# Kernel tuning notes

Hardware: AMD Instinct MI355X
Metric: run time of the kernel (lower is better)

## Reference

```python
import jax, jax.numpy as jnp
import numpy as np

P, N, C, F = 3, 50000, 5, 68   # planes, nodes/plane, classes, in+node feats
E = 150000                     # edges/plane
EF, NF = 64, 64                # edge_features, node_features

def setup_inputs() -> dict:
    key = jax.random.key(0)
    ks = jax.random.split(key, 10)
    s = 0.1
    return {
        "x": jax.random.normal(ks[0], (P, N, C, F), jnp.float32),
        "edge_index": jax.random.randint(ks[1], (P, 2, E), 0, N, jnp.int64),
        "ew1": s * jax.random.normal(ks[2], (P, C, 2 * F, EF), jnp.float32),
        "eb1": s * jax.random.normal(ks[3], (P, C, EF), jnp.float32),
        "ew2": s * jax.random.normal(ks[4], (P, C, EF, 1), jnp.float32),
        "eb2": s * jax.random.normal(ks[5], (P, C, 1), jnp.float32),
        "nw1": s * jax.random.normal(ks[6], (P, C, 2 * F, NF), jnp.float32),
        "nb1": s * jax.random.normal(ks[7], (P, C, NF), jnp.float32),
        "nw2": s * jax.random.normal(ks[8], (P, C, NF, NF), jnp.float32),
        "nb2": s * jax.random.normal(ks[9], (P, C, NF), jnp.float32),
    }

def _plane(x, ei, ew1, eb1, ew2, eb2, nw1, nb1, nw2, nb2):
    # x: [N, C, F]; ei: [2, E]
    src, dst = ei[0], ei[1]
    x_j = x[src]                                   # [E, C, F] (source)
    x_i = x[dst]                                   # [E, C, F] (target)
    # edge net input is detached in the original module
    e_in = jax.lax.stop_gradient(jnp.concatenate([x_i, x_j], axis=-1))  # [E, C, 2F]
    h = jnp.tanh(jnp.einsum('ecf,cfo->eco', e_in, ew1) + eb1)           # [E, C, EF]
    logit = jnp.einsum('ecf,cfo->eco', h, ew2) + eb2                    # [E, C, 1]
    w = jax.nn.softmax(logit, axis=1)              # softmax over classes
    msg = w * x_j                                  # [E, C, F]
    aggr = jax.ops.segment_sum(msg, dst, num_segments=x.shape[0])       # [N, C, F]
    u_in = jnp.concatenate([x, aggr], axis=-1)     # [N, C, 2F]
    h2 = jnp.tanh(jnp.einsum('ncf,cfo->nco', u_in, nw1) + nb1)          # [N, C, NF]
    return jnp.tanh(jnp.einsum('ncf,cfo->nco', h2, nw2) + nb2)          # [N, C, NF]

def reference(x, edge_index, ew1, eb1, ew2, eb2, nw1, nb1, nw2, nb2):
    return jax.vmap(_plane)(x, edge_index, ew1, eb1, ew2, eb2, nw1, nb1, nw2, nb2)
```

## Files before the change

kernel.cpp:

```cpp
#include <hip/hip_runtime.h>
#include <hip/hip_fp16.h>
#include <math.h>

typedef unsigned int uint;
typedef __fp16 half2_t __attribute__((ext_vector_type(2)));
typedef _Float16 v8h __attribute__((ext_vector_type(8)));
typedef _Float16 v4h __attribute__((ext_vector_type(4)));
typedef float f32v4 __attribute__((ext_vector_type(4)));

#define NUM_P 3
#define NUM_N 50000
#define NUM_C 5
#define NUM_E 150000
#define CF 340
#define NB32 1563
#define TE 128
#define EB2 1172
#define TN 128
#define NB128 391
#define SROW 129
#define NSB 196
#define NSBP 50176

#define AH_T   ((size_t)NUM_P * NUM_N * 170)
#define NW1_T  (NUM_P * NUM_C * 68 * 64)
#define NW2_T  (NUM_P * NUM_C * 32 * 64)
#define LG_T   ((size_t)NUM_P * NUM_C * NUM_E)
#define EWB_T  (NUM_P * NUM_C * 2 * 4 * 640)

__device__ __forceinline__ float fast_tanh(float x) {
    float a = __expf(2.0f * x);
    float t = __builtin_amdgcn_rcpf(a + 1.0f);
    return fmaf(-2.0f, t, 1.0f);
}

__device__ __forceinline__ float dot2f(half2_t a, half2_t b, float c) {
#if __has_builtin(__builtin_amdgcn_fdot2)
    return __builtin_amdgcn_fdot2(a, b, c, false);
#else
    return fmaf((float)a[0], (float)b[0], fmaf((float)a[1], (float)b[1], c));
#endif
}

__device__ __forceinline__ half2_t bc(uint u) { return __builtin_bit_cast(half2_t, u); }

__device__ __forceinline__ uint pk2(float a, float b) {
    half2_t h = __builtin_amdgcn_cvt_pkrtz(a, b);
    return __builtin_bit_cast(uint, h);
}

__global__ __launch_bounds__(256) void convert_x_kernel(
    const float4* __restrict__ x4, uint* __restrict__ xh,
    uint* __restrict__ xn, int write_xn)
{
    __shared__ uint lds[32 * 170];
    const int nb = blockIdx.x % NB32;
    const int p  = blockIdx.x / NB32;
    const int n0 = nb * 32;
    const int nvalid = (n0 + 32 <= NUM_N) ? 32 : (NUM_N - n0);
    const int t = threadIdx.x;

    const float4* src = x4 + ((size_t)p * NUM_N + n0) * 85;
    const int nf4 = nvalid * 85;
    #pragma unroll
    for (int it = 0; it < 11; ++it) {
        const int i = t + it * 256;
        if (i < nf4) {
            const float4 v = src[i];
            lds[2 * i]     = pk2(v.x, v.y);
            lds[2 * i + 1] = pk2(v.z, v.w);
        }
    }
    __syncthreads();

    const int nq = nvalid * 34;
    #pragma unroll 1
    for (int c = 0; c < NUM_C; ++c) {
        uint* dst = xh + ((size_t)(p * NUM_C + c) * NUM_N + n0) * 34;
        #pragma unroll
        for (int it = 0; it < 5; ++it) {
            const int i = t + it * 256;
            if (i < nq) {
                const int nl = i / 34, j = i - nl * 34;
                dst[i] = lds[nl * 170 + c * 34 + j];
            }
        }
    }

    if (write_xn) {
        uint* dstn = xn + ((size_t)p * NUM_N + n0) * 170;
        const int tot = nvalid * 170;
        #pragma unroll
        for (int it = 0; it < 22; ++it) {
            const int i = t + it * 256;
            if (i < tot) dstn[i] = lds[i];
        }
    }
}

__global__ __launch_bounds__(256) void pack_pairs_kernel(
    const float* __restrict__ in, uint* __restrict__ outp, int total)
{
    int i = blockIdx.x * 256 + threadIdx.x;
    if (i >= total) return;
    int t = i >> 6, o = i & 63;
    outp[i] = pk2(in[t * 128 + o], in[t * 128 + 64 + o]);
}

__global__ __launch_bounds__(256) void pack_edge_mfma_kernel(
    const float* __restrict__ ew1, uint* __restrict__ ewb)
{
    int i = blockIdx.x * 256 + threadIdx.x;
    if (i >= EWB_T) return;
    int g    = i / 5120;
    int rem  = i - g * 5120;
    int s    = rem / 2560;
    int rem2 = rem - s * 2560;
    int nt   = rem2 / 640;
    int u    = rem2 - nt * 640;

    int f0, o; bool valid;
    if (u < 512) {
        int kt = u >> 8, uu = u & 255;
        int lane = uu >> 2, pp = uu & 3;
        f0 = kt * 32 + (lane >> 4) * 8 + 2 * pp;
        o  = nt * 16 + (lane & 15);
        valid = true;
    } else {
        int uu = u - 512;
        int lane = uu >> 1, pp = uu & 1;
        f0 = 64 + (lane >> 4) * 4 + 2 * pp;
        o  = nt * 16 + (lane & 15);
        valid = ((lane >> 4) == 0);
    }
    float w0 = 0.f, w1 = 0.f;
    if (valid) {
        int f = s * 68 + f0;
        w0 = ew1[((size_t)g * 136 + f) * 64 + o];
        w1 = ew1[((size_t)g * 136 + f + 1) * 64 + o];
    }
    ewb[i] = pk2(w0, w1);
}

__global__ __launch_bounds__(128) void edge_mfma_kernel(
    const uint*  __restrict__ xh,
    const int*   __restrict__ ei,
    const uint*  __restrict__ ewb,
    const float* __restrict__ eb1,
    const float* __restrict__ ew2,
    const float* __restrict__ eb2,
    float*       __restrict__ logits)
{
    __shared__ uint smem[TE * 40];
    __shared__ int  ids[2][TE];

    const int g    = blockIdx.x / EB2;
    const int blk  = blockIdx.x - g * EB2;
    const int p    = g / NUM_C;
    const int e0   = blk * TE;
    const int t    = threadIdx.x;
    const int lane = t & 63;
    const int wv   = t >> 6;
    const int col  = lane & 15;
    const int G    = lane >> 4;

    {
        const int e  = e0 + t;
        const int ec = (e < NUM_E) ? e : (NUM_E - 1);
        ids[0][t] = ei[(p * 2 + 0) * NUM_E + ec];
        ids[1][t] = ei[(p * 2 + 1) * NUM_E + ec];
    }
    {
        const uint2 z = make_uint2(0u, 0u);
        *(uint2*)&smem[t * 40 + 34] = z;
        *(uint2*)&smem[t * 40 + 36] = z;
        *(uint2*)&smem[t * 40 + 38] = z;
    }

    const uint* slice = xh + (size_t)g * NUM_N * 34;

    float b1v[4], w2v[4];
    #pragma unroll
    for (int nt = 0; nt < 4; ++nt) {
        b1v[nt] = eb1[g * 64 + nt * 16 + col];
        w2v[nt] = ew2[g * 64 + nt * 16 + col];
    }

    f32v4 acc[4][4];
    #pragma unroll
    for (int m = 0; m < 4; ++m)
        #pragma unroll
        for (int nt = 0; nt < 4; ++nt) {
            f32v4 a = {b1v[nt], b1v[nt], b1v[nt], b1v[nt]};
            acc[m][nt] = a;
        }
    __syncthreads();

    #pragma unroll 1
    for (int side = 0; side < 2; ++side) {
        const int* idr = ids[1 - side];
        #pragma unroll
        for (int k = 0; k < 17; ++k) {
            const int i2 = t + TE * k;
            const int e  = i2 / 17, j2 = i2 - e * 17;
            const uint2 v = *(const uint2*)(slice + (size_t)idr[e] * 34 + 2 * j2);
            *(uint2*)&smem[e * 40 + 2 * j2] = v;
        }
        __syncthreads();

        const uint* wb = ewb + (size_t)((g * 2 + side) * 4) * 640;
        v8h B0[4], B1[4]; v4h B2[4];
        #pragma unroll
        for (int nt = 0; nt < 4; ++nt) {
            const uint* fb = wb + nt * 640;
            B0[nt] = __builtin_bit_cast(v8h, *(const uint4*)(fb + lane * 4));
            B1[nt] = __builtin_bit_cast(v8h, *(const uint4*)(fb + 256 + lane * 4));
            B2[nt] = __builtin_bit_cast(v4h, *(const uint2*)(fb + 512 + lane * 2));
        }

        #pragma unroll
        for (int m = 0; m < 4; ++m) {
            const uint* rp = &smem[(wv * 64 + m * 16 + col) * 40];
            const v8h A0 = __builtin_bit_cast(v8h, *(const uint4*)(rp + G * 4));
            const v8h A1 = __builtin_bit_cast(v8h, *(const uint4*)(rp + 16 + G * 4));
            const v4h A2 = __builtin_bit_cast(v4h, *(const uint2*)(rp + 32 + G * 2));
            #pragma unroll
            for (int nt = 0; nt < 4; ++nt) {
                acc[m][nt] = __builtin_amdgcn_mfma_f32_16x16x32_f16(A0, B0[nt], acc[m][nt], 0, 0, 0);
                acc[m][nt] = __builtin_amdgcn_mfma_f32_16x16x32_f16(A1, B1[nt], acc[m][nt], 0, 0, 0);
                acc[m][nt] = __builtin_amdgcn_mfma_f32_16x16x16f16(A2, B2[nt], acc[m][nt], 0, 0, 0);
            }
        }
        __syncthreads();
    }

    float* elds = (float*)smem;
    #pragma unroll
    for (int m = 0; m < 4; ++m) {
        #pragma unroll
        for (int r = 0; r < 4; ++r) {
            float part = 0.f;
            #pragma unroll
            for (int nt = 0; nt < 4; ++nt)
                part = fmaf(w2v[nt], fast_tanh(acc[m][nt][r]), part);
            elds[(wv * 64 + m * 16 + G * 4 + r) * 20 + col] = part;
        }
    }
    const float4 s0 = *(const float4*)&elds[t * 20 + 0];
    const float4 s1 = *(const float4*)&elds[t * 20 + 4];
    const float4 s2 = *(const float4*)&elds[t * 20 + 8];
    const float4 s3 = *(const float4*)&elds[t * 20 + 12];
    float lg = ((s0.x + s0.y) + (s0.z + s0.w)) + ((s1.x + s1.y) + (s1.z + s1.w))
             + ((s2.x + s2.y) + (s2.z + s2.w)) + ((s3.x + s3.y) + (s3.z + s3.w))
             + eb2[g];
    if (e0 + t < NUM_E) logits[(size_t)g * NUM_E + e0 + t] = lg;
}

__global__ __launch_bounds__(256) void deg_kernel(
    const int* __restrict__ ei, int* __restrict__ deg)
{
    const int i = blockIdx.x * 256 + threadIdx.x;
    if (i >= NUM_P * NUM_E) return;
    const int p = i / NUM_E, e = i - p * NUM_E;
    const int dst = ei[(p * 2 + 1) * NUM_E + e];
    atomicAdd(&deg[p * NUM_N + dst], 1);
}

__global__ __launch_bounds__(256) void scan_block_kernel(
    const int* __restrict__ deg, int* __restrict__ intra, int* __restrict__ bsum)
{
    __shared__ int s[256];
    const int blk = blockIdx.x % NSB;
    const int p   = blockIdx.x / NSB;
    const int t   = threadIdx.x;
    const int n   = blk * 256 + t;
    const int d   = (n < NUM_N) ? deg[p * NUM_N + n] : 0;
    s[t] = d;
    __syncthreads();
    #pragma unroll
    for (int o = 1; o < 256; o <<= 1) {
        int v = (t >= o) ? s[t - o] : 0;
        __syncthreads();
        s[t] += v;
        __syncthreads();
    }
    if (n < NUM_N) intra[p * NSBP + n] = s[t] - d;
    if (t == 255) bsum[p * NSB + blk] = s[255];
}

__global__ __launch_bounds__(256) void scan_seg_kernel(
    const int* __restrict__ bsum, int* __restrict__ segoff)
{
    __shared__ int s[256];
    const int t = threadIdx.x;
    #pragma unroll 1
    for (int p = 0; p < NUM_P; ++p) {
        const int b = (t < NSB) ? bsum[p * NSB + t] : 0;
        s[t] = b;
        __syncthreads();
        #pragma unroll
        for (int o = 1; o < 256; o <<= 1) {
            int v = (t >= o) ? s[t - o] : 0;
            __syncthreads();
            s[t] += v;
            __syncthreads();
        }
        if (t < NSB) segoff[p * NSB + t] = s[t] - b;
        __syncthreads();
    }
}

__global__ __launch_bounds__(256) void fill_kernel(
    const int* __restrict__ ei, int* __restrict__ cursor,
    const int* __restrict__ intra, const int* __restrict__ segoff,
    int* __restrict__ csr_src, int* __restrict__ csr_eid)
{
    const int i = blockIdx.x * 256 + threadIdx.x;
    if (i >= NUM_P * NUM_E) return;
    const int p = i / NUM_E, e = i - p * NUM_E;
    const int src = ei[(p * 2 + 0) * NUM_E + e];
    const int dst = ei[(p * 2 + 1) * NUM_E + e];
    const int slot = atomicAdd(&cursor[p * NUM_N + dst], 1);
    const int pos  = segoff[p * NSB + (dst >> 8)] + intra[p * NSBP + dst] + slot;
    csr_src[(size_t)p * NUM_E + pos] = src;
    csr_eid[(size_t)p * NUM_E + pos] = e;
}

__global__ __launch_bounds__(256) void gather_kernel(
    const uint*  __restrict__ xn,
    const float* __restrict__ logits,
    const int*   __restrict__ csr_src,
    const int*   __restrict__ csr_eid,
    const int*   __restrict__ deg,
    const int*   __restrict__ intra,
    const int*   __restrict__ segoff,
    uint*        __restrict__ aggr)
{
    const int wslot = threadIdx.x >> 6;
    const int lane  = threadIdx.x & 63;
    const int gw = blockIdx.x * 4 + wslot;
    const int p  = gw / NUM_N;
    const int n  = gw - p * NUM_N;

    const int dg   = deg[p * NUM_N + n];
    const int off0 = segoff[p * NSB + (n >> 8)] + intra[p * NSBP + n];

    const int q1 = lane + 64, q2 = lane + 128;
    const int c0 = lane / 34;
    const int c1 = q1 / 34;
    const int c2 = q2 / 34;

    float a0 = 0.f, a1 = 0.f, a2 = 0.f, a3 = 0.f, a4 = 0.f, a5 = 0.f;

    #pragma unroll 1
    for (int d = 0; d < dg; ++d) {
        const int src = csr_src[(size_t)p * NUM_E + off0 + d];
        const int e   = csr_eid[(size_t)p * NUM_E + off0 + d];

        float l[NUM_C];
        #pragma unroll
        for (int c = 0; c < NUM_C; ++c)
            l[c] = logits[(size_t)(p * NUM_C + c) * NUM_E + e];
        float m = l[0];
        #pragma unroll
        for (int c = 1; c < NUM_C; ++c) m = fmaxf(m, l[c]);
        float s = 0.f;
        #pragma unroll
        for (int c = 0; c < NUM_C; ++c) { l[c] = __expf(l[c] - m); s += l[c]; }
        const float inv = __builtin_amdgcn_rcpf(s);
        const float wt0 = l[0] * inv, wt1 = l[1] * inv, wt2 = l[2] * inv,
                    wt3 = l[3] * inv, wt4 = l[4] * inv;

        const float wa = (c0 == 0) ? wt0 : wt1;
        const float wb = (c1 == 1) ? wt1 : (c1 == 2) ? wt2 : wt3;
        const float wc = (c2 == 3) ? wt3 : wt4;

        const uint* row = xn + (size_t)(p * NUM_N + src) * 170;
        const uint u0 = row[lane];
        const uint u1 = row[q1];
        const uint u2 = (lane < 42) ? row[q2] : 0u;
        const half2_t h0 = bc(u0), h1 = bc(u1), h2 = bc(u2);
        a0 = fmaf(wa, (float)h0[0], a0);
        a1 = fmaf(wa, (float)h0[1], a1);
        a2 = fmaf(wb, (float)h1[0], a2);
        a3 = fmaf(wb, (float)h1[1], a3);
        a4 = fmaf(wc, (float)h2[0], a4);
        a5 = fmaf(wc, (float)h2[1], a5);
    }

    const int i0 = lane - c0 * 34;
    const int i1 = q1 - c1 * 34;
    const int i2 = q2 - c2 * 34;
    aggr[((size_t)(p * NUM_C + c0) * NUM_N + n) * 34 + i0] = pk2(a0, a1);
    aggr[((size_t)(p * NUM_C + c1) * NUM_N + n) * 34 + i1] = pk2(a2, a3);
    if (lane < 42)
        aggr[((size_t)(p * NUM_C + c2) * NUM_N + n) * 34 + i2] = pk2(a4, a5);
}

__global__ __launch_bounds__(256) void edge_scatter_kernel(
    const uint*  __restrict__ xh,
    const int*   __restrict__ ei,
    const float* __restrict__ logits,
    uint*        __restrict__ aggr)
{
    const int wslot = threadIdx.x >> 6;
    const int lane  = threadIdx.x & 63;
    const int gw    = blockIdx.x * 4 + wslot;
    const int p     = gw / NUM_E;
    const int e     = gw - p * NUM_E;

    const int src = ei[(p * 2 + 0) * NUM_E + e];
    const int dst = ei[(p * 2 + 1) * NUM_E + e];

    float l[NUM_C];
    #pragma unroll
    for (int c = 0; c < NUM_C; ++c)
        l[c] = logits[(size_t)(p * NUM_C + c) * NUM_E + e];
    float m = l[0];
    #pragma unroll
    for (int c = 1; c < NUM_C; ++c) m = fmaxf(m, l[c]);
    float s = 0.f;
    #pragma unroll
    for (int c = 0; c < NUM_C; ++c) { l[c] = __expf(l[c] - m); s += l[c]; }
    const float inv = __builtin_amdgcn_rcpf(s);
    const float wt0 = l[0] * inv, wt1 = l[1] * inv, wt2 = l[2] * inv,
                wt3 = l[3] * inv, wt4 = l[4] * inv;

    #pragma unroll
    for (int k = 0; k < 3; ++k) {
        const int q = lane + 64 * k;
        if (q < 170) {
            const int c   = q / 34;
            const int idx = q - c * 34;
            const float wv = (c == 0) ? wt0 : (c == 1) ? wt1 : (c == 2) ? wt2
                           : (c == 3) ? wt3 : wt4;
            const uint xv = xh[((size_t)(p * NUM_C + c) * NUM_N + src) * 34 + idx];
            half2_t mv = __builtin_amdgcn_cvt_pkrtz(wv, wv) * bc(xv);
            uint* ap = aggr + ((size_t)(p * NUM_C + c) * NUM_N + dst) * 34 + idx;
            unsafeAtomicAdd((__half2*)ap, __builtin_bit_cast(__half2, mv));
        }
    }
}

__device__ __forceinline__ void dot_side(const uint* __restrict__ xp,
                                         const uint* __restrict__ wp,
                                         float acc[64])
{
    uint2 cur = *(const uint2*)(xp);
    #pragma unroll 1
    for (int j = 0; j < 17; ++j) {
        const int jn = (j < 16) ? (j + 1) : 16;
        const uint2 nxt = *(const uint2*)(xp + jn * 2);
        const half2_t a0 = bc(cur.x);
        const half2_t a1 = bc(cur.y);
        const uint* w0 = wp + (2 * j) * 64;
        #pragma unroll
        for (int o = 0; o < 64; ++o)
            acc[o] = dot2f(a0, bc(w0[o]), acc[o]);
        const uint* w1 = w0 + 64;
        #pragma unroll
        for (int o = 0; o < 64; ++o)
            acc[o] = dot2f(a1, bc(w1[o]), acc[o]);
        cur = nxt;
    }
}

__device__ __forceinline__ void dot_side_f32(const float* __restrict__ xf,
                                             const uint* __restrict__ wp,
                                             float acc[64])
{
    float4 cur = *(const float4*)(xf);
    #pragma unroll 1
    for (int j = 0; j < 17; ++j) {
        const int jn = (j < 16) ? (j + 1) : 16;
        const float4 nxt = *(const float4*)(xf + jn * 4);
        const half2_t a0 = __builtin_amdgcn_cvt_pkrtz(cur.x, cur.y);
        const half2_t a1 = __builtin_amdgcn_cvt_pkrtz(cur.z, cur.w);
        const uint* w0 = wp + (2 * j) * 64;
        #pragma unroll
        for (int o = 0; o < 64; ++o)
            acc[o] = dot2f(a0, bc(w0[o]), acc[o]);
        const uint* w1 = w0 + 64;
        #pragma unroll
        for (int o = 0; o < 64; ++o)
            acc[o] = dot2f(a1, bc(w1[o]), acc[o]);
        cur = nxt;
    }
}

__global__ __launch_bounds__(128) void node_kernel(
    const float* __restrict__ x,
    const uint*  __restrict__ xh,
    const uint*  __restrict__ aggr,
    const uint*  __restrict__ nwp,
    const uint*  __restrict__ n2p,
    const float* __restrict__ nb1,
    const float* __restrict__ nb2,
    float*       __restrict__ out,
    int use_xh)
{
    __shared__ uint buf[34][SROW];

    const int g   = blockIdx.x / NB128;
    const int blk = blockIdx.x - g * NB128;
    const int p   = g / NUM_C;
    const int c   = g - p * NUM_C;
    const int n0  = blk * TN;
    const int t   = threadIdx.x;
    const int nvalid = (n0 + TN <= NUM_N) ? TN : (NUM_N - n0);
    const int lim2 = nvalid * 17;

    float acc[64];
    const float* b1 = nb1 + g * 64;
    #pragma unroll
    for (int o4 = 0; o4 < 64; o4 += 4) {
        const float4 bv = *(const float4*)(b1 + o4);
        acc[o4] = bv.x; acc[o4 + 1] = bv.y; acc[o4 + 2] = bv.z; acc[o4 + 3] = bv.w;
    }
    const uint* wg = nwp + (size_t)g * 68 * 64;

    if (use_xh) {
        const uint* srcp = xh + ((size_t)g * NUM_N + n0) * 34;
        #pragma unroll
        for (int k = 0; k < 17; ++k) {
            const int i2  = t + TN * k;
            const int i2c = (i2 < lim2) ? i2 : (lim2 - 1);
            const uint2 v = *(const uint2*)(srcp + 2 * i2c);
            const int nl = i2 / 17, j2 = i2 - nl * 17;
            buf[2 * j2][nl]     = v.x;
            buf[2 * j2 + 1][nl] = v.y;
        }
    } else {
        #pragma unroll
        for (int k = 0; k < 34; ++k) {
            const int i  = t + TN * k;
            const int nl = i / 34, j = i - nl * 34;
            const int nn = (nl < nvalid) ? (n0 + nl) : n0;
            const float2 v = *(const float2*)(x + ((size_t)p * NUM_N + nn) * CF
                                              + c * 68 + 2 * j);
            buf[j][nl] = pk2(v.x, v.y);
        }
    }
    __syncthreads();
    #pragma unroll 1
    for (int j = 0; j < 34; ++j) {
        const half2_t a = bc(buf[j][t]);
        const uint* w = wg + j * 64;
        #pragma unroll
        for (int o = 0; o < 64; ++o) acc[o] = dot2f(a, bc(w[o]), acc[o]);
    }
    __syncthreads();

    {
        const uint* srcp = aggr + ((size_t)g * NUM_N + n0) * 34;
        #pragma unroll
        for (int k = 0; k < 17; ++k) {
            const int i2  = t + TN * k;
            const int i2c = (i2 < lim2) ? i2 : (lim2 - 1);
            const uint2 v = *(const uint2*)(srcp + 2 * i2c);
            const int nl = i2 / 17, j2 = i2 - nl * 17;
            buf[2 * j2][nl]     = v.x;
            buf[2 * j2 + 1][nl] = v.y;
        }
    }
    __syncthreads();
    #pragma unroll 1
    for (int j = 0; j < 34; ++j) {
        const half2_t a = bc(buf[j][t]);
        const uint* w = wg + (34 + j) * 64;
        #pragma unroll
        for (int o = 0; o < 64; ++o) acc[o] = dot2f(a, bc(w[o]), acc[o]);
    }

    uint h2p[32];
    #pragma unroll
    for (int f2 = 0; f2 < 32; ++f2)
        h2p[f2] = pk2(fast_tanh(acc[2 * f2]), fast_tanh(acc[2 * f2 + 1]));

    const float* b2 = nb2 + g * 64;
    float acc2[64];
    #pragma unroll
    for (int o4 = 0; o4 < 64; o4 += 4) {
        const float4 bv = *(const float4*)(b2 + o4);
        acc2[o4] = bv.x; acc2[o4 + 1] = bv.y; acc2[o4 + 2] = bv.z; acc2[o4 + 3] = bv.w;
    }
    const uint* w2g = n2p + (size_t)g * 32 * 64;
    #pragma unroll
    for (int f2 = 0; f2 < 32; ++f2) {
        const half2_t hv = bc(h2p[f2]);
        const uint* wr = w2g + f2 * 64;
        #pragma unroll
        for (int o = 0; o < 64; ++o)
            acc2[o] = dot2f(hv, bc(wr[o]), acc2[o]);
    }

    if (t < nvalid) {
        float* op = out + ((size_t)(p * NUM_N + n0 + t) * NUM_C + c) * 64;
        #pragma unroll
        for (int o4 = 0; o4 < 64; o4 += 4) {
            float4 ov;
            ov.x = fast_tanh(acc2[o4 + 0]);
            ov.y = fast_tanh(acc2[o4 + 1]);
            ov.z = fast_tanh(acc2[o4 + 2]);
            ov.w = fast_tanh(acc2[o4 + 3]);
            *(float4*)(op + o4) = ov;
        }
    }
}

extern "C" void kernel_launch(void* const* d_in, const int* in_sizes, int n_in,
                              void* d_out, int out_size, void* d_ws, size_t ws_size,
                              hipStream_t stream)
{
    (void)in_sizes; (void)n_in; (void)out_size;

    const float* x   = (const float*)d_in[0];
    const int*   ei  = (const int*)  d_in[1];
    const float* ew1 = (const float*)d_in[2];
    const float* eb1 = (const float*)d_in[3];
    const float* ew2 = (const float*)d_in[4];
    const float* eb2 = (const float*)d_in[5];
    const float* nw1 = (const float*)d_in[6];
    const float* nb1 = (const float*)d_in[7];
    const float* nw2 = (const float*)d_in[8];
    const float* nb2 = (const float*)d_in[9];
    float*       out = (float*)d_out;

    uint* ws     = (uint*)d_ws;
    uint* aggr_h = ws;
    uint* nwp    = ws + AH_T;
    uint* n2p    = nwp + NW1_T;
    const size_t o_xh = AH_T + NW1_T + NW2_T;
    const bool fits = ws_size >= (o_xh + AH_T) * sizeof(uint);
    uint*  xh     = fits ? (ws + o_xh) : (uint*)d_out;
    uint*  xn     = (uint*)d_out;
    float* logits = (float*)((uint*)d_out + AH_T);
    uint*  ewb    = (uint*)d_out + AH_T + LG_T;

    int* ibase   = (int*)(ewb + EWB_T);
    int* deg     = ibase;
    int* cursor  = ibase + NUM_P * NUM_N;
    int* intra   = cursor + NUM_P * NUM_N;
    int* bsum    = intra + NUM_P * NSBP;
    int* segoff  = bsum + NUM_P * NSB;
    int* csr_src = segoff + NUM_P * NSB;
    int* csr_eid = csr_src + NUM_P * NUM_E;

    convert_x_kernel<<<NUM_P * NB32, 256, 0, stream>>>(
        (const float4*)x, xh, xn, fits ? 1 : 0);
    pack_edge_mfma_kernel<<<(EWB_T + 255) / 256, 256, 0, stream>>>(ew1, ewb);
    pack_pairs_kernel<<<(NW1_T + 255) / 256, 256, 0, stream>>>(nw1, nwp, NW1_T);
    pack_pairs_kernel<<<(NW2_T + 255) / 256, 256, 0, stream>>>(nw2, n2p, NW2_T);

    edge_mfma_kernel<<<NUM_P * NUM_C * EB2, 128, 0, stream>>>(
        xh, ei, ewb, eb1, ew2, eb2, logits);

    if (fits) {
        (void)hipMemsetAsync(ibase, 0, (size_t)2 * NUM_P * NUM_N * sizeof(int), stream);
        const int egrid = (NUM_P * NUM_E + 255) / 256;
        deg_kernel<<<egrid, 256, 0, stream>>>(ei, deg);
        scan_block_kernel<<<NUM_P * NSB, 256, 0, stream>>>(deg, intra, bsum);
        scan_seg_kernel<<<1, 256, 0, stream>>>(bsum, segoff);
        fill_kernel<<<egrid, 256, 0, stream>>>(ei, cursor, intra, segoff,
                                               csr_src, csr_eid);
        gather_kernel<<<(NUM_P * NUM_N) / 4, 256, 0, stream>>>(
            xn, logits, csr_src, csr_eid, deg, intra, segoff, aggr_h);
    } else {
        (void)hipMemsetAsync(aggr_h, 0, AH_T * sizeof(uint), stream);
        edge_scatter_kernel<<<(NUM_P * NUM_E) / 4, 256, 0, stream>>>(
            xh, ei, logits, aggr_h);
    }

    node_kernel<<<NUM_P * NUM_C * NB128, 128, 0, stream>>>(
        x, xh, aggr_h, nwp, n2p, nb1, nb2, out, fits ? 1 : 0);
}
```

Baseline: 668.7 us.

## Port node MLP to MFMA matrix instructions with LDS-staged tiles

Adds a node kernel that computes both node-MLP layers with f16 MFMA instructions instead of per-thread dot2 loops. Node features and aggregates are staged in padded LDS rows, the first layer's hidden activations are written back to LDS as f16, and the output goes through an LDS transpose for coalesced stores. The goal is to turn the compute-bound scalar dot products into matrix-core throughput. In exchange it adds LDS traffic and extra synchronisation, and the new path only runs when the CSR path is selected.

```diff
diff --git a/kernel.cpp b/kernel.cpp
--- a/kernel.cpp
+++ b/kernel.cpp
@@ -49,6 +49,11 @@
     return __builtin_bit_cast(uint, h);
 }
 
+__device__ __forceinline__ v8h mk8(uint a, uint b, uint c, uint d) {
+    uint4 u; u.x = a; u.y = b; u.z = c; u.w = d;
+    return __builtin_bit_cast(v8h, u);
+}
+
 __global__ __launch_bounds__(256) void convert_x_kernel(
     const float4* __restrict__ x4, uint* __restrict__ xh,
     uint* __restrict__ xn, int write_xn)
@@ -442,6 +447,164 @@
     }
 }
 
+__global__ __launch_bounds__(128) void node_mfma_kernel(
+    const uint*  __restrict__ xh,
+    const uint*  __restrict__ aggr,
+    const uint*  __restrict__ nwp,
+    const uint*  __restrict__ n2p,
+    const float* __restrict__ nb1,
+    const float* __restrict__ nb2,
+    float*       __restrict__ out)
+{
+    __shared__ uint smem[TN * 40];
+
+    const int g    = blockIdx.x / NB128;
+    const int blk  = blockIdx.x - g * NB128;
+    const int p    = g / NUM_C;
+    const int c    = g - p * NUM_C;
+    const int n0   = blk * TN;
+    const int t    = threadIdx.x;
+    const int lane = t & 63;
+    const int wv   = t >> 6;
+    const int col  = lane & 15;
+    const int G    = lane >> 4;
+    const int nvalid = (n0 + TN <= NUM_N) ? TN : (NUM_N - n0);
+    const int lim2   = nvalid * 17;
+
+    {
+        const uint2 z = make_uint2(0u, 0u);
+        *(uint2*)&smem[t * 40 + 34] = z;
+        *(uint2*)&smem[t * 40 + 36] = z;
+        *(uint2*)&smem[t * 40 + 38] = z;
+    }
+
+    const uint* wgp = nwp + (size_t)g * 68 * 64;
+
+    float b1v[4];
+    #pragma unroll
+    for (int nt = 0; nt < 4; ++nt) b1v[nt] = nb1[g * 64 + nt * 16 + col];
+
+    f32v4 acc[4][4];
+    #pragma unroll
+    for (int m = 0; m < 4; ++m)
+        #pragma unroll
+        for (int nt = 0; nt < 4; ++nt) {
+            f32v4 a = {b1v[nt], b1v[nt], b1v[nt], b1v[nt]};
+            acc[m][nt] = a;
+        }
+
+    #pragma unroll 1
+    for (int side = 0; side < 2; ++side) {
+        const uint* srcp = (side == 0 ? xh : aggr) + ((size_t)g * NUM_N + n0) * 34;
+        #pragma unroll
+        for (int k = 0; k < 17; ++k) {
+            const int i2  = t + TN * k;
+            const int i2c = (i2 < lim2) ? i2 : (lim2 - 1);
+            const uint2 v = *(const uint2*)(srcp + 2 * i2c);
+            const int nl = i2 / 17, j2 = i2 - nl * 17;
+            *(uint2*)&smem[nl * 40 + 2 * j2] = v;
+        }
+        __syncthreads();
+
+        v8h B0[4], B1[4]; v4h B2[4];
+        #pragma unroll
+        for (int nt = 0; nt < 4; ++nt) {
+            const int oc = nt * 16 + col;
+            const int r0 = side * 34 + G * 4;
+            B0[nt] = mk8(wgp[(r0 + 0) * 64 + oc], wgp[(r0 + 1) * 64 + oc],
+                         wgp[(r0 + 2) * 64 + oc], wgp[(r0 + 3) * 64 + oc]);
+            const int r1 = r0 + 16;
+            B1[nt] = mk8(wgp[(r1 + 0) * 64 + oc], wgp[(r1 + 1) * 64 + oc],
+                         wgp[(r1 + 2) * 64 + oc], wgp[(r1 + 3) * 64 + oc]);
+            uint b2a = (G == 0) ? wgp[(side * 34 + 32) * 64 + oc] : 0u;
+            uint b2b = (G == 0) ? wgp[(side * 34 + 33) * 64 + oc] : 0u;
+            uint2 u2; u2.x = b2a; u2.y = b2b;
+            B2[nt] = __builtin_bit_cast(v4h, u2);
+        }
+
+        #pragma unroll
+        for (int m = 0; m < 4; ++m) {
+            const uint* rp = &smem[(wv * 64 + m * 16 + col) * 40];
+            const v8h A0 = __builtin_bit_cast(v8h, *(const uint4*)(rp + G * 4));
+            const v8h A1 = __builtin_bit_cast(v8h, *(const uint4*)(rp + 16 + G * 4));
+            const v4h A2 = __builtin_bit_cast(v4h, *(const uint2*)(rp + 32 + G * 2));
+            #pragma unroll
+            for (int nt = 0; nt < 4; ++nt) {
+                acc[m][nt] = __builtin_amdgcn_mfma_f32_16x16x32_f16(A0, B0[nt], acc[m][nt], 0, 0, 0);
+                acc[m][nt] = __builtin_amdgcn_mfma_f32_16x16x32_f16(A1, B1[nt], acc[m][nt], 0, 0, 0);
+                acc[m][nt] = __builtin_amdgcn_mfma_f32_16x16x16f16(A2, B2[nt], acc[m][nt], 0, 0, 0);
+            }
+        }
+        __syncthreads();
+    }
+
+    _Float16* hl = (_Float16*)smem;
+    #pragma unroll
+    for (int m = 0; m < 4; ++m)
+        #pragma unroll
+        for (int nt = 0; nt < 4; ++nt)
+            #pragma unroll
+            for (int r = 0; r < 4; ++r)
+                hl[(wv * 64 + m * 16 + G * 4 + r) * 72 + nt * 16 + col] =
+                    (_Float16)fast_tanh(acc[m][nt][r]);
+
+    const uint* w2p = n2p + (size_t)g * 32 * 64;
+    float b2v[4];
+    #pragma unroll
+    for (int nt = 0; nt < 4; ++nt) b2v[nt] = nb2[g * 64 + nt * 16 + col];
+
+    f32v4 acc2[4][4];
+    #pragma unroll
+    for (int m = 0; m < 4; ++m)
+        #pragma unroll
+        for (int nt = 0; nt < 4; ++nt) {
+            f32v4 a = {b2v[nt], b2v[nt], b2v[nt], b2v[nt]};
+            acc2[m][nt] = a;
+        }
+
+    v8h C0[4], C1[4];
+    #pragma unroll
+    for (int nt = 0; nt < 4; ++nt) {
+        const int oc = nt * 16 + col;
+        C0[nt] = mk8(w2p[(G * 4 + 0) * 64 + oc], w2p[(G * 4 + 1) * 64 + oc],
+                     w2p[(G * 4 + 2) * 64 + oc], w2p[(G * 4 + 3) * 64 + oc]);
+        C1[nt] = mk8(w2p[(16 + G * 4 + 0) * 64 + oc], w2p[(16 + G * 4 + 1) * 64 + oc],
+                     w2p[(16 + G * 4 + 2) * 64 + oc], w2p[(16 + G * 4 + 3) * 64 + oc]);
+    }
+
+    #pragma unroll
+    for (int m = 0; m < 4; ++m) {
+        const uint* rp = &smem[(wv * 64 + m * 16 + col) * 36];
+        const v8h A0 = __builtin_bit_cast(v8h, *(const uint4*)(rp + G * 4));
+        const v8h A1 = __builtin_bit_cast(v8h, *(const uint4*)(rp + 16 + G * 4));
+        #pragma unroll
+        for (int nt = 0; nt < 4; ++nt) {
+            acc2[m][nt] = __builtin_amdgcn_mfma_f32_16x16x32_f16(A0, C0[nt], acc2[m][nt], 0, 0, 0);
+            acc2[m][nt] = __builtin_amdgcn_mfma_f32_16x16x32_f16(A1, C1[nt], acc2[m][nt], 0, 0, 0);
+        }
+    }
+    __syncthreads();
+
+    float* elds = (float*)smem;
+    #pragma unroll
+    for (int pass = 0; pass < 2; ++pass) {
+        #pragma unroll
+        for (int m = 0; m < 4; ++m)
+            #pragma unroll
+            for (int r = 0; r < 4; ++r) {
+                const int row = wv * 64 + m * 16 + G * 4 + r;
+                elds[row * 40 + col]      = fast_tanh(acc2[m][2 * pass][r]);
+                elds[row * 40 + 16 + col] = fast_tanh(acc2[m][2 * pass + 1][r]);
+            }
+        if (t < nvalid) {
+            float* op = out + ((size_t)(p * NUM_N + n0 + t) * NUM_C + c) * 64 + pass * 32;
+            #pragma unroll
+            for (int q = 0; q < 8; ++q)
+                *(float4*)(op + q * 4) = *(const float4*)&elds[t * 40 + q * 4];
+        }
+    }
+}
+
 __device__ __forceinline__ void dot_side(const uint* __restrict__ xp,
                                          const uint* __restrict__ wp,
                                          float acc[64])
@@ -465,39 +628,14 @@
     }
 }
 
-__device__ __forceinline__ void dot_side_f32(const float* __restrict__ xf,
-                                             const uint* __restrict__ wp,
-                                             float acc[64])
-{
-    float4 cur = *(const float4*)(xf);
-    #pragma unroll 1
-    for (int j = 0; j < 17; ++j) {
-        const int jn = (j < 16) ? (j + 1) : 16;
-        const float4 nxt = *(const float4*)(xf + jn * 4);
-        const half2_t a0 = __builtin_amdgcn_cvt_pkrtz(cur.x, cur.y);
-        const half2_t a1 = __builtin_amdgcn_cvt_pkrtz(cur.z, cur.w);
-        const uint* w0 = wp + (2 * j) * 64;
-        #pragma unroll
-        for (int o = 0; o < 64; ++o)
-            acc[o] = dot2f(a0, bc(w0[o]), acc[o]);
-        const uint* w1 = w0 + 64;
-        #pragma unroll
-        for (int o = 0; o < 64; ++o)
-            acc[o] = dot2f(a1, bc(w1[o]), acc[o]);
-        cur = nxt;
-    }
-}
-
 __global__ __launch_bounds__(128) void node_kernel(
     const float* __restrict__ x,
-    const uint*  __restrict__ xh,
     const uint*  __restrict__ aggr,
     const uint*  __restrict__ nwp,
     const uint*  __restrict__ n2p,
     const float* __restrict__ nb1,
     const float* __restrict__ nb2,
-    float*       __restrict__ out,
-    int use_xh)
+    float*       __restrict__ out)
 {
     __shared__ uint buf[34][SROW];
 
@@ -519,27 +657,14 @@
     }
     const uint* wg = nwp + (size_t)g * 68 * 64;
 
-    if (use_xh) {
-        const uint* srcp = xh + ((size_t)g * NUM_N + n0) * 34;
-        #pragma unroll
-        for (int k = 0; k < 17; ++k) {
-            const int i2  = t + TN * k;
-            const int i2c = (i2 < lim2) ? i2 : (lim2 - 1);
-            const uint2 v = *(const uint2*)(srcp + 2 * i2c);
-            const int nl = i2 / 17, j2 = i2 - nl * 17;
-            buf[2 * j2][nl]     = v.x;
-            buf[2 * j2 + 1][nl] = v.y;
-        }
-    } else {
-        #pragma unroll
-        for (int k = 0; k < 34; ++k) {
-            const int i  = t + TN * k;
-            const int nl = i / 34, j = i - nl * 34;
-            const int nn = (nl < nvalid) ? (n0 + nl) : n0;
-            const float2 v = *(const float2*)(x + ((size_t)p * NUM_N + nn) * CF
-                                              + c * 68 + 2 * j);
-            buf[j][nl] = pk2(v.x, v.y);
-        }
+    #pragma unroll
+    for (int k = 0; k < 34; ++k) {
+        const int i  = t + TN * k;
+        const int nl = i / 34, j = i - nl * 34;
+        const int nn = (nl < nvalid) ? (n0 + nl) : n0;
+        const float2 v = *(const float2*)(x + ((size_t)p * NUM_N + nn) * CF
+                                          + c * 68 + 2 * j);
+        buf[j][nl] = pk2(v.x, v.y);
     }
     __syncthreads();
     #pragma unroll 1
@@ -665,12 +790,13 @@
                                                csr_src, csr_eid);
         gather_kernel<<<(NUM_P * NUM_N) / 4, 256, 0, stream>>>(
             xn, logits, csr_src, csr_eid, deg, intra, segoff, aggr_h);
+        node_mfma_kernel<<<NUM_P * NUM_C * NB128, 128, 0, stream>>>(
+            xh, aggr_h, nwp, n2p, nb1, nb2, out);
     } else {
         (void)hipMemsetAsync(aggr_h, 0, AH_T * sizeof(uint), stream);
         edge_scatter_kernel<<<(NUM_P * NUM_E) / 4, 256, 0, stream>>>(
             xh, ei, logits, aggr_h);
-    }
-
-    node_kernel<<<NUM_P * NUM_C * NB128, 128, 0, stream>>>(
-        x, xh, aggr_h, nwp, n2p, nb1, nb2, out, fits ? 1 : 0);
-}
+        node_kernel<<<NUM_P * NUM_C * NB128, 128, 0, stream>>>(
+            x, aggr_h, nwp, n2p, nb1, nb2, out);
+    }
+}
```

Result: faster. 638.1 us (-4.6%).
